# Kernel tuning notes

Measured on AMD Instinct MI355X. Metric: run time of the kernel, lower is better.

The kernel has to match this reference:

```python
import jax, jax.numpy as jnp
import numpy as np
from jax import lax

B, CIN, HIN, WIN = 8, 64, 256, 256
DIM, HEADS, KD, NHKD, D, DH, POS = 128, 8, 8, 64, 16, 128, 16
CQKV = 2 * NHKD + DH  # 256
DN = ('NCHW', 'OIHW', 'NCHW')


def _cbn(x, w, s, b):
    # 1x1 conv (no bias) + eval-mode BN fused into per-channel scale/bias
    y = jnp.einsum('bchw,oc->bohw', x, w)
    return y * s[:, None, None] + b[:, None, None]


def _interp(pos, n):
    # F.interpolate(mode='linear', align_corners=False) == half-pixel linear resize
    return jax.image.resize(pos, (1, pos.shape[1], n), method='linear')


def setup_inputs() -> dict:
    key = jax.random.key(0)
    ks = jax.random.split(key, 40)
    i = [0]
    def nk():
        i[0] += 1
        return ks[i[0] - 1]
    def w(shp, s=0.05):
        return jax.random.normal(nk(), shp, jnp.float32) * s
    def bn(c):
        return (1.0 + 0.1 * jax.random.normal(nk(), (c,), jnp.float32),
                0.1 * jax.random.normal(nk(), (c,), jnp.float32))
    inp = {}
    inp['x'] = jax.random.normal(nk(), (B, CIN, HIN, WIN), jnp.float32)
    inp['bn1_s'], inp['bn1_b'] = bn(DIM)
    inp['fc1_w'] = w((DIM, DIM, 3, 3))
    inp['fc1_b'] = w((DIM,))
    inp['wq'] = w((NHKD, DIM)); inp['bnq_s'], inp['bnq_b'] = bn(NHKD)
    inp['wk'] = w((NHKD, DIM)); inp['bnk_s'], inp['bnk_b'] = bn(NHKD)
    inp['wv'] = w((DH, DIM)); inp['bnv_s'], inp['bnv_b'] = bn(DH)
    inp['pos_rq'] = w((1, NHKD, POS), 1.0)
    inp['pos_rk'] = w((1, NHKD, POS), 1.0)
    inp['pos_cq'] = w((1, NHKD, POS), 1.0)
    inp['pos_ck'] = w((1, NHKD, POS), 1.0)
    inp['wrow'] = w((DH, DH)); inp['bnrow_s'], inp['bnrow_b'] = bn(DH)
    inp['wcol'] = w((DH, DH)); inp['bncol_s'], inp['bncol_b'] = bn(DH)
    inp['wproj'] = w((DIM, DH)); inp['bnproj_s'], inp['bnproj_b'] = bn(DIM)
    inp['wdw'] = w((CQKV, 1, 3, 3)); inp['bndw_s'], inp['bndw_b'] = bn(CQKV)
    inp['wpw'] = w((DIM, CQKV)); inp['bnpw_s'], inp['bnpw_b'] = bn(DIM)
    return inp


def reference(x, bn1_s, bn1_b, fc1_w, fc1_b,
              wq, bnq_s, bnq_b, wk, bnk_s, bnk_b, wv, bnv_s, bnv_b,
              pos_rq, pos_rk, pos_cq, pos_ck,
              wrow, bnrow_s, bnrow_b, wcol, bncol_s, bncol_b,
              wproj, bnproj_s, bnproj_b,
              wdw, bndw_s, bndw_b, wpw, bnpw_s, bnpw_b):
    pad = [(0, 0), (0, 0), (1, 1), (1, 1)]
    # AvgPool2d(3,2,1) with count_include_pad=True, MaxPool2d(3,2,1)
    y_avg = lax.reduce_window(x, 0.0, lax.add, (1, 1, 3, 3), (1, 1, 2, 2), pad) / 9.0
    y_max = lax.reduce_window(x, -jnp.inf, lax.max, (1, 1, 3, 3), (1, 1, 2, 2), pad)
    y = jnp.concatenate([y_avg, y_max], axis=1)  # [B, DIM, H, W]
    # fc1: BN -> Mish -> Conv3x3 (bias) -> Dropout(eval=identity)
    y = y * bn1_s[:, None, None] + bn1_b[:, None, None]
    y = y * jnp.tanh(jax.nn.softplus(y))
    y = lax.conv_general_dilated(y, fc1_w, (1, 1), [(1, 1), (1, 1)], dimension_numbers=DN)
    y = y + fc1_b[:, None, None]
    Bq, _, H, W = y.shape
    # Attention
    q = _cbn(y, wq, bnq_s, bnq_b)   # [B, NHKD, H, W]
    k = _cbn(y, wk, bnk_s, bnk_b)   # [B, NHKD, H, W]
    v = _cbn(y, wv, bnv_s, bnv_b)   # [B, DH, H, W]
    qkv = jnp.concatenate([q, k, v], axis=1)  # [B, CQKV, H, W]
    qkv = lax.conv_general_dilated(qkv, wdw, (1, 1), [(1, 1), (1, 1)],
                                   dimension_numbers=DN, feature_group_count=CQKV)
    qkv = jax.nn.relu(qkv * bndw_s[:, None, None] + bndw_b[:, None, None])
    qkv = _cbn(qkv, wpw, bnpw_s, bnpw_b)  # [B, DIM, H, W]
    scale = KD ** -0.5
    # row attention (squeeze W)
    qr = (q.mean(-1) + _interp(pos_rq, H)).reshape(Bq, HEADS, KD, H)
    kr = (k.mean(-1) + _interp(pos_rk, H)).reshape(Bq, HEADS, KD, H)
    vr = v.mean(-1).reshape(Bq, HEADS, D, H)
    attn_r = jax.nn.softmax(jnp.einsum('bhki,bhkj->bhij', qr, kr) * scale, axis=-1)
    xr = jnp.einsum('bhij,bhdj->bhdi', attn_r, vr).reshape(Bq, DH, H, 1)
    xr = _cbn(jax.nn.relu(xr), wrow, bnrow_s, bnrow_b)
    # column attention (squeeze H)
    qc = (q.mean(-2) + _interp(pos_cq, W)).reshape(Bq, HEADS, KD, W)
    kc = (k.mean(-2) + _interp(pos_ck, W)).reshape(Bq, HEADS, KD, W)
    vc = v.mean(-2).reshape(Bq, HEADS, D, W)
    attn_c = jax.nn.softmax(jnp.einsum('bhki,bhkj->bhij', qc, kc) * scale, axis=-1)
    xc = jnp.einsum('bhij,bhdj->bhdi', attn_c, vc).reshape(Bq, DH, 1, W)
    xc = _cbn(jax.nn.relu(xc), wcol, bncol_s, bncol_b)
    xx = v + xr + xc
    xx = _cbn(jax.nn.relu(xx), wproj, bnproj_s, bnproj_b)
    # h_sigmoid gate * qkv
    return jnp.clip(xx + 3.0, 0.0, 6.0) / 6.0 * qkv
```

## Files before the change

### kernel.cpp

```cpp
#include <hip/hip_runtime.h>
#include <math.h>

#define S 16384
#define HW 128

typedef __attribute__((ext_vector_type(8))) short short8;
typedef __attribute__((ext_vector_type(4))) float f32x4;

__device__ __forceinline__ float mishf(float t) {
    float sp = (t > 20.0f) ? t : __logf(1.0f + __expf(t));
    float e2 = __expf(-2.0f * sp);
    return t * (1.0f - e2) * __builtin_amdgcn_rcpf(1.0f + e2);
}
__device__ __forceinline__ short f2bf(float f) {
    unsigned u = __float_as_uint(f);
    unsigned r = (u + 0x7FFFu + ((u >> 16) & 1u)) >> 16;
    return (short)r;
}
__device__ __forceinline__ float bf2f(short s) {
    unsigned u = ((unsigned)(unsigned short)s) << 16;
    return __uint_as_float(u);
}
__device__ __forceinline__ unsigned packhl(float v) {
    short h = f2bf(v);
    short l = f2bf(v - bf2f(h));
    return (unsigned)(unsigned short)h | ((unsigned)(unsigned short)l << 16);
}
__device__ __forceinline__ void gl_lds16(const void* g, void* l) {
    __builtin_amdgcn_global_load_lds(
        (const __attribute__((address_space(1))) unsigned int*)g,
        (__attribute__((address_space(3))) unsigned int*)l, 16, 0, 0);
}
__device__ __forceinline__ short8 lds_frag(const char* base, int a) {
    int p = a ^ (((a >> 8) & 7) << 4);
    return *(const short8*)(base + p);
}
__device__ __forceinline__ short8 lds_frag128(const char* base, int a) {
    int p = a ^ (((a >> 7) & 7) << 4);
    return *(const short8*)(base + p);
}
__device__ __forceinline__ int swz128(int a) { return a ^ (((a >> 7) & 7) << 4); }
#define MFMA(a, b, c) __builtin_amdgcn_mfma_f32_16x16x32_bf16(a, b, c, 0, 0, 0)

__global__ void prep_kernel(const float* __restrict__ wq, const float* __restrict__ wk, const float* __restrict__ wv,
                            const float* __restrict__ bnq_s, const float* __restrict__ bnq_b,
                            const float* __restrict__ bnk_s, const float* __restrict__ bnk_b,
                            const float* __restrict__ bnv_s, const float* __restrict__ bnv_b,
                            const float* __restrict__ wpw, const float* __restrict__ wproj,
                            const float* __restrict__ wrow, const float* __restrict__ wcol,
                            const float* __restrict__ fc1_w, const float* __restrict__ wdw,
                            short* __restrict__ wqkv_h,
                            float* __restrict__ sqkv, float* __restrict__ bqkv,
                            short* __restrict__ wpw_h,
                            short* __restrict__ wproj_h,
                            float* __restrict__ wrowT, float* __restrict__ wcolT,
                            short* __restrict__ wch,
                            float* __restrict__ wdwT,
                            short* __restrict__ t0ph, short* __restrict__ t0pl) {
    int tid = blockIdx.x * 256 + threadIdx.x;
    if (tid < 256 * 128) {
        int oc = tid >> 7, ic = tid & 127;
        float w = (oc < 64) ? wq[oc * 128 + ic]
                : (oc < 128) ? wk[(oc - 64) * 128 + ic]
                : wv[(oc - 128) * 128 + ic];
        wqkv_h[tid] = f2bf(w);
    }
    if (tid < 256) {
        sqkv[tid] = (tid < 64) ? bnq_s[tid] : (tid < 128) ? bnk_s[tid - 64] : bnv_s[tid - 128];
        bqkv[tid] = (tid < 64) ? bnq_b[tid] : (tid < 128) ? bnk_b[tid - 64] : bnv_b[tid - 128];
    }
    if (tid < 128 * 256) {
        wpw_h[tid] = f2bf(wpw[tid]);
    }
    if (tid < 128 * 128) {
        wproj_h[tid] = f2bf(wproj[tid]);
        int ic = tid >> 7, oc = tid & 127;
        wrowT[tid] = wrow[oc * 128 + ic];
        wcolT[tid] = wcol[oc * 128 + ic];
    }
    if (tid < 9 * 128 * 128) {
        int tap = tid >> 14;
        int oc = (tid >> 7) & 127;
        int ic = tid & 127;
        wch[tid] = f2bf(fc1_w[(oc * 128 + ic) * 9 + tap]);
    }
    if (tid < 9 * 256) {
        int tap = tid / 256, c = tid % 256;
        wdwT[tap * 256 + c] = wdw[c * 9 + tap];
    }
    if (tid < 132096) {
        int bb = tid / 16512;
        int rem = tid - bb * 16512;
        int part = rem / 8256;
        int e = rem - part * 8256;
        short* p = part ? t0pl : t0ph;
        size_t ib = (size_t)bb * 130 * 130 * 128;
        short8 z = (short8){0, 0, 0, 0, 0, 0, 0, 0};
        if (e < 4160) {
            int row = (e < 2080) ? 0 : 129;
            int off = (e % 2080) * 8;
            *(short8*)(p + ib + (size_t)row * 130 * 128 + off) = z;
        } else {
            int e2 = e - 4160;
            int row = 1 + (e2 >> 5);
            int side = (e2 >> 4) & 1;
            int off = (e2 & 15) * 8;
            *(short8*)(p + ib + ((size_t)row * 130 + (side ? 129 : 0)) * 128 + off) = z;
        }
    }
}

__global__ __launch_bounds__(256) void pool_kernel(const float* __restrict__ x,
                                                   const float* __restrict__ s1, const float* __restrict__ b1,
                                                   short* __restrict__ t0ph, short* __restrict__ t0pl) {
    __shared__ unsigned ot[64][132];
    int bx = blockIdx.x;
    int b = blockIdx.y;
    int h = bx >> 1, wh = bx & 1;
    int t = threadIdx.x;
    int wp = t & 31;
    int c8 = t >> 5;
    int w0 = wh * 64 + wp * 2;
    for (int cs = 0; cs < 8; ++cs) {
        int c = cs * 8 + c8;
        const float* xp = x + (size_t)(b * 64 + c) * 65536;
        float vs[3][5], vm[3][5];
        #pragma unroll
        for (int kh = 0; kh < 3; ++kh) {
            int ih = 2 * h + kh - 1;
            bool hok = (unsigned)ih < 256u;
            #pragma unroll
            for (int j = 0; j < 5; ++j) {
                int iw = 2 * w0 - 1 + j;
                bool ok = hok && (unsigned)iw < 256u;
                float v = ok ? xp[ih * 256 + iw] : 0.f;
                vs[kh][j] = ok ? v : 0.f;
                vm[kh][j] = ok ? v : -INFINITY;
            }
        }
        #pragma unroll
        for (int o = 0; o < 2; ++o) {
            float sum = 0.f, mx = -INFINITY;
            #pragma unroll
            for (int kh = 0; kh < 3; ++kh)
                #pragma unroll
                for (int kw = 0; kw < 3; ++kw) {
                    sum += vs[kh][kw + 2 * o];
                    mx = fmaxf(mx, vm[kh][kw + 2 * o]);
                }
            float ta = mishf((sum * (1.f / 9.f)) * s1[c] + b1[c]);
            float tm = mishf(mx * s1[64 + c] + b1[64 + c]);
            ot[wp * 2 + o][c] = packhl(ta);
            ot[wp * 2 + o][64 + c] = packhl(tm);
        }
    }
    __syncthreads();
    size_t rowbase = ((size_t)(b * 130 + h + 1) * 130 + 1 + wh * 64) * 128;
    short* oph = t0ph + rowbase;
    short* opl = t0pl + rowbase;
    for (int idx = t; idx < 64 * 16; idx += 256) {
        int wloc = idx >> 4, co = idx & 15;
        short8 hv, lv;
        #pragma unroll
        for (int j = 0; j < 8; ++j) {
            unsigned u = ot[wloc][co * 8 + j];
            hv[j] = (short)(u & 0xFFFFu);
            lv[j] = (short)(u >> 16);
        }
        *(short8*)(oph + wloc * 128 + co * 8) = hv;
        *(short8*)(opl + wloc * 128 + co * 8) = lv;
    }
}

__global__ __launch_bounds__(512) void convqkv_mfma(const short* __restrict__ t0ph,
                                                    const short* __restrict__ t0pl,
                                                    const short* __restrict__ wch,
                                                    const float* __restrict__ fb,
                                                    const short* __restrict__ wqkv_h,
                                                    const float* __restrict__ sc, const float* __restrict__ bi,
                                                    short* __restrict__ qh, float* __restrict__ rowmean) {
    __shared__ char sm[69632];
    char* smh = sm;
    char* sml = sm + 33792;
    float* rsum = (float*)(sm + 67584);
    int flat = blockIdx.x;
    int b = flat & 7;
    int h = flat >> 3;
    int tid = threadIdx.x, lane = tid & 63, wid = tid >> 6;
    int l15 = lane & 15, l4 = lane >> 4;
    int wrc = wid >> 2;
    int wcc = wid & 3;
    int spbc = wrc * 64 + l15;
    int ocbc = wcc * 32 + l15;
    f32x4 acc[4][2];
    #pragma unroll
    for (int m = 0; m < 4; ++m)
        #pragma unroll
        for (int n = 0; n < 2; ++n) acc[m][n] = (f32x4){0.f, 0.f, 0.f, 0.f};
    for (int kh = 0; kh < 3; ++kh) {
        __syncthreads();
        const char* gh = (const char*)(t0ph + ((size_t)(b * 130 + h + kh) * 130) * 128);
        const char* gl = (const char*)(t0pl + ((size_t)(b * 130 + h + kh) * 130) * 128);
        #pragma unroll
        for (int it = 0; it < 5; ++it) {
            int idx = it * 512 + tid;
            if (idx < 2080) {
                int dl = idx * 16;
                int srcoff = dl ^ (((dl >> 8) & 7) << 4);
                gl_lds16(gh + srcoff, smh + dl);
                gl_lds16(gl + srcoff, sml + dl);
            }
        }
        __syncthreads();
        #pragma unroll
        for (int kw = 0; kw < 3; ++kw) {
            const short* wbh = wch + (size_t)(kh * 3 + kw) * 16384;
            #pragma unroll
            for (int ks = 0; ks < 4; ++ks) {
                int kb = ks * 64 + l4 * 16;
                int kws = ks * 32 + l4 * 8;
                short8 ah[4], bh[2];
                #pragma unroll
                for (int m = 0; m < 4; ++m)
                    ah[m] = lds_frag(smh, ((spbc + m * 16 + kw) << 8) + kb);
                #pragma unroll
                for (int n = 0; n < 2; ++n)
                    bh[n] = *(const short8*)(wbh + (ocbc + n * 16) * 128 + kws);
                #pragma unroll
                for (int m = 0; m < 4; ++m)
                    #pragma unroll
                    for (int n = 0; n < 2; ++n)
                        acc[m][n] = MFMA(ah[m], bh[n], acc[m][n]);
                short8 al[4];
                #pragma unroll
                for (int m = 0; m < 4; ++m)
                    al[m] = lds_frag(sml, ((spbc + m * 16 + kw) << 8) + kb);
                #pragma unroll
                for (int m = 0; m < 4; ++m)
                    #pragma unroll
                    for (int n = 0; n < 2; ++n)
                        acc[m][n] = MFMA(al[m], bh[n], acc[m][n]);
            }
        }
    }
    float fbv[2];
    #pragma unroll
    for (int n = 0; n < 2; ++n) fbv[n] = fb[wcc * 32 + n * 16 + l15];
    rsum[tid] = 0.f;
    __syncthreads();
    short* ahi = (short*)sm;
    short* alo = (short*)(sm + 33792);
    #pragma unroll
    for (int m = 0; m < 4; ++m)
        #pragma unroll
        for (int n = 0; n < 2; ++n)
            #pragma unroll
            for (int r = 0; r < 4; ++r) {
                int px = wrc * 64 + m * 16 + l4 * 4 + r;
                int ocl = wcc * 32 + n * 16 + l15;
                unsigned u = packhl(acc[m][n][r] + fbv[n]);
                ahi[px * 132 + ocl] = (short)(u & 0xFFFFu);
                alo[px * 132 + ocl] = (short)(u >> 16);
            }
    __syncthreads();
    int spbq = wrc * 64 + l15;
    int ocbq = wcc * 64 + l15;
    f32x4 aq[4][4];
    #pragma unroll
    for (int m = 0; m < 4; ++m)
        #pragma unroll
        for (int n = 0; n < 4; ++n) aq[m][n] = (f32x4){0.f, 0.f, 0.f, 0.f};
    #pragma unroll
    for (int ks = 0; ks < 4; ++ks) {
        int k0 = ks * 32 + l4 * 8;
        short8 ah[4], bh[4];
        #pragma unroll
        for (int m = 0; m < 4; ++m) ah[m] = *(const short8*)(ahi + (spbq + m * 16) * 132 + k0);
        #pragma unroll
        for (int n = 0; n < 4; ++n) bh[n] = *(const short8*)(wqkv_h + (size_t)(ocbq + n * 16) * 128 + k0);
        #pragma unroll
        for (int m = 0; m < 4; ++m)
            #pragma unroll
            for (int n = 0; n < 4; ++n) aq[m][n] = MFMA(ah[m], bh[n], aq[m][n]);
        short8 al[4];
        #pragma unroll
        for (int m = 0; m < 4; ++m) al[m] = *(const short8*)(alo + (spbq + m * 16) * 132 + k0);
        #pragma unroll
        for (int m = 0; m < 4; ++m)
            #pragma unroll
            for (int n = 0; n < 4; ++n) aq[m][n] = MFMA(al[m], bh[n], aq[m][n]);
    }
    #pragma unroll
    for (int n = 0; n < 4; ++n) {
        float v = 0.f;
        #pragma unroll
        for (int m = 0; m < 4; ++m)
            #pragma unroll
            for (int r = 0; r < 4; ++r) v += aq[m][n][r];
        v += __shfl_xor(v, 16);
        v += __shfl_xor(v, 32);
        if (l4 == 0) rsum[wrc * 256 + wcc * 64 + n * 16 + l15] = v;
    }
    float s4[4], b4[4];
    #pragma unroll
    for (int n = 0; n < 4; ++n) {
        s4[n] = sc[wcc * 64 + n * 16 + l15];
        b4[n] = bi[wcc * 64 + n * 16 + l15];
    }
    short* rowout = qh + ((size_t)(b * 128 + h) * 128) * 256;
    #pragma unroll
    for (int m = 0; m < 4; ++m)
        #pragma unroll
        for (int n = 0; n < 4; ++n)
            #pragma unroll
            for (int r = 0; r < 4; ++r) {
                int px = wrc * 64 + m * 16 + l4 * 4 + r;
                int oc = wcc * 64 + n * 16 + l15;
                rowout[px * 256 + oc] = f2bf(aq[m][n][r] * s4[n] + b4[n]);
            }
    __syncthreads();
    if (tid < 256)
        rowmean[((size_t)b * 256 + tid) * 128 + h] =
            (rsum[tid] + rsum[256 + tid]) * sc[tid] * (1.f / 128.f) + bi[tid];
}

__global__ __launch_bounds__(256) void colmean_kernel(const short* __restrict__ qh,
                                                      float* __restrict__ colmean) {
    __shared__ float red[8][256];
    int blk = blockIdx.x;
    int b = blk & 7, w = blk >> 3;
    int tid = threadIdx.x;
    int c8g = tid & 31;
    int hs = tid >> 5;
    float a8[8];
    #pragma unroll
    for (int k = 0; k < 8; ++k) a8[k] = 0.f;
    for (int j = 0; j < 16; ++j) {
        int h = hs * 16 + j;
        short8 v = *(const short8*)(qh + ((size_t)((b * 128 + h) * 128 + w)) * 256 + c8g * 8);
        #pragma unroll
        for (int k = 0; k < 8; ++k) a8[k] += bf2f(v[k]);
    }
    #pragma unroll
    for (int k = 0; k < 8; ++k) red[hs][c8g * 8 + k] = a8[k];
    __syncthreads();
    int c = tid;
    float s = 0.f;
    #pragma unroll
    for (int q = 0; q < 8; ++q) s += red[q][c];
    colmean[((size_t)b * 256 + c) * 128 + w] = s * (1.f / 128.f);
}

__global__ __launch_bounds__(512) void dwpw_mfma(const short* __restrict__ qh,
                                                 const float* __restrict__ wdwT,
                                                 const float* __restrict__ ds, const float* __restrict__ db,
                                                 const short* __restrict__ wpw_h,
                                                 const float* __restrict__ sc, const float* __restrict__ bi,
                                                 float* __restrict__ qb) {
    __shared__ char sm[32768];
    char* smh = sm;
    char* sml = sm + 16384;
    int flat = blockIdx.x;
    int b = flat & 7, h = flat >> 3;
    int tid = threadIdx.x, lane = tid & 63, wid = tid >> 6;
    int wr = wid >> 2, wc = wid & 3;
    int l15 = lane & 15, l4 = lane >> 4;
    int spb = wr * 64 + l15;
    int ocb = wc * 32 + l15;
    int wdw_ = tid >> 3;
    int c8t = tid & 7;
    f32x4 acc[4][2];
    #pragma unroll
    for (int m = 0; m < 4; ++m)
        #pragma unroll
        for (int n = 0; n < 2; ++n) acc[m][n] = (f32x4){0.f, 0.f, 0.f, 0.f};

    #pragma unroll 1
    for (int kc = 0; kc < 4; ++kc) {
        __syncthreads();
        int cbase = kc * 64 + c8t * 8;
        #pragma unroll 1
        for (int i = 0; i < 2; ++i) {
            int w = wdw_ * 2 + i;
            float acc8[8];
            #pragma unroll
            for (int k = 0; k < 8; ++k) acc8[k] = 0.f;
            #pragma unroll
            for (int kh = 0; kh < 3; ++kh) {
                int ih = h + kh - 1;
                if ((unsigned)ih >= 128u) continue;
                #pragma unroll
                for (int kw = 0; kw < 3; ++kw) {
                    int iw = w + kw - 1;
                    if ((unsigned)iw >= 128u) continue;
                    short8 v = *(const short8*)(qh + ((size_t)((b * 128 + ih) * 128 + iw)) * 256 + cbase);
                    const float* wp = wdwT + (kh * 3 + kw) * 256 + cbase;
                    #pragma unroll
                    for (int k = 0; k < 8; ++k)
                        acc8[k] += wp[k] * bf2f(v[k]);
                }
            }
            short8 hv, lv;
            #pragma unroll
            for (int k = 0; k < 8; ++k) {
                float v = fmaxf(acc8[k] * ds[cbase + k] + db[cbase + k], 0.f);
                unsigned u = packhl(v);
                hv[k] = (short)(u & 0xFFFFu);
                lv[k] = (short)(u >> 16);
            }
            int a = swz128(w * 128 + c8t * 16);
            *(short8*)(smh + a) = hv;
            *(short8*)(sml + a) = lv;
        }
        __syncthreads();
        #pragma unroll
        for (int ks = 0; ks < 2; ++ks) {
            int kb = ks * 64 + l4 * 16;
            int kws = kc * 64 + ks * 32 + l4 * 8;
            short8 ah[4], bh[2];
            #pragma unroll
            for (int m = 0; m < 4; ++m) ah[m] = lds_frag128(smh, (spb + m * 16) * 128 + kb);
            #pragma unroll
            for (int n = 0; n < 2; ++n) bh[n] = *(const short8*)(wpw_h + (ocb + n * 16) * 256 + kws);
            #pragma unroll
            for (int m = 0; m < 4; ++m)
                #pragma unroll
                for (int n = 0; n < 2; ++n) acc[m][n] = MFMA(ah[m], bh[n], acc[m][n]);
            short8 al[4];
            #pragma unroll
            for (int m = 0; m < 4; ++m) al[m] = lds_frag128(sml, (spb + m * 16) * 128 + kb);
            #pragma unroll
            for (int m = 0; m < 4; ++m)
                #pragma unroll
                for (int n = 0; n < 2; ++n) acc[m][n] = MFMA(al[m], bh[n], acc[m][n]);
        }
    }
    float s4[2], b4[2];
    #pragma unroll
    for (int n = 0; n < 2; ++n) {
        s4[n] = sc[wc * 32 + n * 16 + l15];
        b4[n] = bi[wc * 32 + n * 16 + l15];
    }
    float* rowout = qb + ((size_t)(b * 128 + h) * 128) * 128;
    #pragma unroll
    for (int m = 0; m < 4; ++m)
        #pragma unroll
        for (int n = 0; n < 2; ++n)
            #pragma unroll
            for (int r = 0; r < 4; ++r) {
                int px = wr * 64 + m * 16 + l4 * 4 + r;
                int oc = wc * 32 + n * 16 + l15;
                rowout[px * 128 + oc] = acc[m][n][r] * s4[n] + b4[n];
            }
}

__global__ __launch_bounds__(128) void attn_kernel(const float* __restrict__ rowmean,
                                                   const float* __restrict__ colmean,
                                                   const float* __restrict__ pos_rq, const float* __restrict__ pos_rk,
                                                   const float* __restrict__ pos_cq, const float* __restrict__ pos_ck,
                                                   float* __restrict__ xr_act, float* __restrict__ xc_act) {
    __shared__ float qr[8][128], kr[8][128], vr[16][128];
    int iscol = blockIdx.x >> 6;
    int sub = blockIdx.x & 63;
    int b = sub >> 3, head = sub & 7;
    const float* meanbuf = iscol ? colmean : rowmean;
    const float* posq = iscol ? pos_cq : pos_rq;
    const float* posk = iscol ? pos_ck : pos_rk;
    float* xact = iscol ? xc_act : xr_act;
    int i = threadIdx.x;
    float src = (i + 0.5f) * 0.125f - 0.5f;
    src = fmaxf(src, 0.f);
    int i0 = (int)src;
    if (i0 > 15) i0 = 15;
    float f = src - (float)i0;
    int i1 = (i0 + 1 > 15) ? 15 : i0 + 1;
    const float* mb = meanbuf + (size_t)b * 256 * 128;
    for (int kd = 0; kd < 8; ++kd) {
        int cq = head * 8 + kd;
        qr[kd][i] = mb[cq * 128 + i] + posq[cq * 16 + i0] * (1.f - f) + posq[cq * 16 + i1] * f;
        kr[kd][i] = mb[(64 + cq) * 128 + i] + posk[cq * 16 + i0] * (1.f - f) + posk[cq * 16 + i1] * f;
    }
    for (int d = 0; d < 16; ++d)
        vr[d][i] = mb[(128 + head * 16 + d) * 128 + i];
    __syncthreads();
    float qreg[8];
    #pragma unroll
    for (int kd = 0; kd < 8; ++kd) qreg[kd] = qr[kd][i];
    const float scale = 0.35355339059327373f;
    float m = -INFINITY;
    for (int j = 0; j < 128; ++j) {
        float sj = 0.f;
        #pragma unroll
        for (int kd = 0; kd < 8; ++kd) sj += qreg[kd] * kr[kd][j];
        m = fmaxf(m, sj * scale);
    }
    float denom = 0.f;
    float acc[16];
    #pragma unroll
    for (int d = 0; d < 16; ++d) acc[d] = 0.f;
    for (int j = 0; j < 128; ++j) {
        float sj = 0.f;
        #pragma unroll
        for (int kd = 0; kd < 8; ++kd) sj += qreg[kd] * kr[kd][j];
        float pj = __expf(sj * scale - m);
        denom += pj;
        #pragma unroll
        for (int d = 0; d < 16; ++d) acc[d] += pj * vr[d][j];
    }
    float inv = __builtin_amdgcn_rcpf(denom);
    float* xp = xact + ((size_t)b * 128 + head * 16) * 128;
    for (int d = 0; d < 16; ++d)
        xp[d * 128 + i] = fmaxf(acc[d] * inv, 0.f);
}

__global__ __launch_bounds__(256) void rc_conv_kernel(const float* __restrict__ xr_act, const float* __restrict__ xc_act,
                                                      const float* __restrict__ wrowT, const float* __restrict__ wcolT,
                                                      const float* __restrict__ rs, const float* __restrict__ rb,
                                                      const float* __restrict__ cs, const float* __restrict__ cb,
                                                      float* __restrict__ xrT, float* __restrict__ xcT) {
    __shared__ float4 lds[128][16];
    int blk = blockIdx.x;
    int iscol = blk >> 4;
    int rem = blk & 15;
    int b = rem >> 1;
    int i0 = (rem & 1) * 64;
    const float* src = iscol ? xc_act : xr_act;
    const float* wT  = iscol ? wcolT : wrowT;
    const float* ss  = iscol ? cs : rs;
    const float* sb  = iscol ? cb : rb;
    float* dst       = iscol ? xcT : xrT;
    int tid = threadIdx.x;
    const float4* src4 = (const float4*)(src + (size_t)b * 16384 + i0);
    for (int idx = tid; idx < 128 * 16; idx += 256) {
        int ic = idx >> 4, q = idx & 15;
        lds[ic][q] = src4[ic * 32 + q];
    }
    __syncthreads();
    int oc = tid & 127, sub = tid >> 7;
    float4 acc[8];
    #pragma unroll
    for (int q = 0; q < 8; ++q) acc[q] = make_float4(0.f, 0.f, 0.f, 0.f);
    for (int ic = 0; ic < 128; ++ic) {
        float w = wT[ic * 128 + oc];
        #pragma unroll
        for (int q = 0; q < 8; ++q) {
            float4 v = lds[ic][sub * 8 + q];
            acc[q].x += w * v.x; acc[q].y += w * v.y;
            acc[q].z += w * v.z; acc[q].w += w * v.w;
        }
    }
    float s = ss[oc], bb = sb[oc];
    int ibase = i0 + sub * 32;
    #pragma unroll
    for (int q = 0; q < 8; ++q) {
        float vv[4] = {acc[q].x, acc[q].y, acc[q].z, acc[q].w};
        #pragma unroll
        for (int r = 0; r < 4; ++r) {
            int i = ibase + q * 4 + r;
            dst[((size_t)b * 128 + i) * 128 + oc] = vv[r] * s + bb;
        }
    }
}

__global__ __launch_bounds__(512) void final_mfma(const short* __restrict__ qh,
                                                  const float* __restrict__ xrT, const float* __restrict__ xcT,
                                                  const short* __restrict__ wproj_h,
                                                  const float* __restrict__ ps, const float* __restrict__ pb,
                                                  const float* __restrict__ qb, float* __restrict__ out) {
    __shared__ char sm[69632];
    short* ahi = (short*)sm;
    short* alo = (short*)(sm + 34816);
    int flat = blockIdx.x;
    int b = flat & 7, h = flat >> 3;
    int tid = threadIdx.x, lane = tid & 63, wid = tid >> 6;
    int wr = wid >> 2, wc = wid & 3;
    int l15 = lane & 15, l4 = lane >> 4;
    int spb = wr * 64 + l15;
    int ocb = wc * 32 + l15;
    for (int i = 0; i < 4; ++i) {
        int idx = tid + i * 512;
        int px = idx >> 4, g = idx & 15;
        short8 v8 = *(const short8*)(qh + ((size_t)((b * 128 + h) * 128 + px)) * 256 + 128 + g * 8);
        const float* xr = xrT + ((size_t)(b * 128 + h)) * 128 + g * 8;
        const float* xc = xcT + ((size_t)(b * 128 + px)) * 128 + g * 8;
        short8 hv, lv;
        #pragma unroll
        for (int k = 0; k < 8; ++k) {
            float v = bf2f(v8[k]) + xr[k] + xc[k];
            v = fmaxf(v, 0.f);
            unsigned u = packhl(v);
            hv[k] = (short)(u & 0xFFFFu);
            lv[k] = (short)(u >> 16);
        }
        *(short8*)(ahi + px * 136 + g * 8) = hv;
        *(short8*)(alo + px * 136 + g * 8) = lv;
    }
    __syncthreads();
    f32x4 acc[4][2];
    #pragma unroll
    for (int m = 0; m < 4; ++m)
        #pragma unroll
        for (int n = 0; n < 2; ++n) acc[m][n] = (f32x4){0.f, 0.f, 0.f, 0.f};
    #pragma unroll
    for (int ks = 0; ks < 4; ++ks) {
        int ko = ks * 32 + l4 * 8;
        short8 ah[4], bh[2];
        #pragma unroll
        for (int m = 0; m < 4; ++m) ah[m] = *(const short8*)(ahi + (spb + m * 16) * 136 + ko);
        #pragma unroll
        for (int n = 0; n < 2; ++n) bh[n] = *(const short8*)(wproj_h + (ocb + n * 16) * 128 + ko);
        #pragma unroll
        for (int m = 0; m < 4; ++m)
            #pragma unroll
            for (int n = 0; n < 2; ++n) acc[m][n] = MFMA(ah[m], bh[n], acc[m][n]);
        short8 al[4];
        #pragma unroll
        for (int m = 0; m < 4; ++m) al[m] = *(const short8*)(alo + (spb + m * 16) * 136 + ko);
        #pragma unroll
        for (int m = 0; m < 4; ++m)
            #pragma unroll
            for (int n = 0; n < 2; ++n) acc[m][n] = MFMA(al[m], bh[n], acc[m][n]);
    }
    float s4[2], b4[2];
    #pragma unroll
    for (int n = 0; n < 2; ++n) {
        s4[n] = ps[wc * 32 + n * 16 + l15];
        b4[n] = pb[wc * 32 + n * 16 + l15];
    }
    float* tr = (float*)sm;
    #pragma unroll 1
    for (int p = 0; p < 2; ++p) {
        __syncthreads();
        if ((wc >> 1) == p) {
            #pragma unroll
            for (int n = 0; n < 2; ++n)
                #pragma unroll
                for (int m = 0; m < 4; ++m)
                    #pragma unroll
                    for (int r = 0; r < 4; ++r) {
                        int px = wr * 64 + m * 16 + l4 * 4 + r;
                        int ocl = (wc & 1) * 32 + n * 16 + l15;
                        int oc = p * 64 + ocl;
                        float val = acc[m][n][r] * s4[n] + b4[n];
                        float hs = fminf(fmaxf(val + 3.f, 0.f), 6.f) * (1.f / 6.f);
                        float g = qb[((size_t)((b * 128 + h) * 128 + px)) * 128 + oc];
                        tr[ocl * 129 + px] = hs * g;
                    }
        }
        __syncthreads();
        int ocl = tid >> 3, q = tid & 7;
        int oc = p * 64 + ocl;
        float* yp = out + (size_t)(b * 128 + oc) * S + h * 128 + q * 16;
        #pragma unroll
        for (int j = 0; j < 16; j += 4) {
            float4 v;
            v.x = tr[ocl * 129 + q * 16 + j];
            v.y = tr[ocl * 129 + q * 16 + j + 1];
            v.z = tr[ocl * 129 + q * 16 + j + 2];
            v.w = tr[ocl * 129 + q * 16 + j + 3];
            *(float4*)(yp + j) = v;
        }
    }
}

extern "C" void kernel_launch(void* const* d_in, const int* in_sizes, int n_in,
                              void* d_out, int out_size, void* d_ws, size_t ws_size,
                              hipStream_t stream) {
    const float* x       = (const float*)d_in[0];
    const float* bn1_s   = (const float*)d_in[1];
    const float* bn1_b   = (const float*)d_in[2];
    const float* fc1_w   = (const float*)d_in[3];
    const float* fc1_b   = (const float*)d_in[4];
    const float* wq      = (const float*)d_in[5];
    const float* bnq_s   = (const float*)d_in[6];
    const float* bnq_b   = (const float*)d_in[7];
    const float* wk      = (const float*)d_in[8];
    const float* bnk_s   = (const float*)d_in[9];
    const float* bnk_b   = (const float*)d_in[10];
    const float* wv      = (const float*)d_in[11];
    const float* bnv_s   = (const float*)d_in[12];
    const float* bnv_b   = (const float*)d_in[13];
    const float* pos_rq  = (const float*)d_in[14];
    const float* pos_rk  = (const float*)d_in[15];
    const float* pos_cq  = (const float*)d_in[16];
    const float* pos_ck  = (const float*)d_in[17];
    const float* wrow    = (const float*)d_in[18];
    const float* bnrow_s = (const float*)d_in[19];
    const float* bnrow_b = (const float*)d_in[20];
    const float* wcol    = (const float*)d_in[21];
    const float* bncol_s = (const float*)d_in[22];
    const float* bncol_b = (const float*)d_in[23];
    const float* wproj   = (const float*)d_in[24];
    const float* bnproj_s= (const float*)d_in[25];
    const float* bnproj_b= (const float*)d_in[26];
    const float* wdw     = (const float*)d_in[27];
    const float* bndw_s  = (const float*)d_in[28];
    const float* bndw_b  = (const float*)d_in[29];
    const float* wpw     = (const float*)d_in[30];
    const float* bnpw_s  = (const float*)d_in[31];
    const float* bnpw_b  = (const float*)d_in[32];

    char* ws = (char*)d_ws;
    short* t0ph  = (short*)(ws);
    short* t0pl  = (short*)(ws + (size_t)34611200);
    short* qkvh  = (short*)(ws + (size_t)136331264);
    float* qkvb  = (float*)(ws + (size_t)270548992);
    char* sp = ws + (size_t)337657856;
    float* rowmean = (float*)sp; sp += 1048576;
    float* colmean = (float*)sp; sp += 1048576;
    float* xr_act  = (float*)sp; sp += 524288;
    float* xc_act  = (float*)sp; sp += 524288;
    float* xrT     = (float*)sp; sp += 524288;
    float* xcT     = (float*)sp; sp += 524288;
    short* wch     = (short*)sp; sp += 294912;
    short* wqkv_h  = (short*)sp; sp += 65536;
    short* wpw_h   = (short*)sp; sp += 65536;
    short* wproj_h = (short*)sp; sp += 32768;
    float* wrowT   = (float*)sp; sp += 65536;
    float* wcolT   = (float*)sp; sp += 65536;
    float* sqkv    = (float*)sp; sp += 1024;
    float* bqkv    = (float*)sp; sp += 1024;
    float* wdwT    = (float*)sp; sp += 9216;

    float* out = (float*)d_out;

    prep_kernel<<<576, 256, 0, stream>>>(wq, wk, wv, bnq_s, bnq_b, bnk_s, bnk_b, bnv_s, bnv_b,
                                         wpw, wproj, wrow, wcol, fc1_w, wdw,
                                         wqkv_h, sqkv, bqkv, wpw_h,
                                         wproj_h, wrowT, wcolT, wch, wdwT,
                                         t0ph, t0pl);
    pool_kernel<<<dim3(256, 8), 256, 0, stream>>>(x, bn1_s, bn1_b, t0ph, t0pl);
    convqkv_mfma<<<1024, 512, 0, stream>>>(t0ph, t0pl, wch, fc1_b,
                                           wqkv_h, sqkv, bqkv, qkvh, rowmean);
    colmean_kernel<<<1024, 256, 0, stream>>>(qkvh, colmean);
    dwpw_mfma<<<1024, 512, 0, stream>>>(qkvh, wdwT, bndw_s, bndw_b,
                                        wpw_h, bnpw_s, bnpw_b, qkvb);
    attn_kernel<<<128, 128, 0, stream>>>(rowmean, colmean, pos_rq, pos_rk, pos_cq, pos_ck,
                                         xr_act, xc_act);
    rc_conv_kernel<<<32, 256, 0, stream>>>(xr_act, xc_act, wrowT, wcolT,
                                           bnrow_s, bnrow_b, bncol_s, bncol_b, xrT, xcT);
    final_mfma<<<1024, 512, 0, stream>>>(qkvh, xrT, xcT, wproj_h,
                                         bnproj_s, bnproj_b, qkvb, out);
}
```

Before: 444.8 us.

## Replace split bf16 hi/lo activations with single fp16 MFMA path

Activations were previously stored as two bf16 halves (hi plus residual lo), and every GEMM ran two MFMA passes to emulate higher precision. The activations and weights now use fp16 with the f16 MFMA instruction, which halves the MFMA count, the activation memory traffic and the LDS footprint in the conv, dwpw and final kernels. The cost is lower precision (fp16 mantissa, limited range), which may hurt accuracy against the fp32 reference.

```diff
diff --git a/kernel.cpp b/kernel.cpp
--- a/kernel.cpp
+++ b/kernel.cpp
@@ -5,6 +5,7 @@
 #define HW 128
 
 typedef __attribute__((ext_vector_type(8))) short short8;
+typedef __attribute__((ext_vector_type(8))) _Float16 half8;
 typedef __attribute__((ext_vector_type(4))) float f32x4;
 
 __device__ __forceinline__ float mishf(float t) {
@@ -12,35 +13,25 @@
     float e2 = __expf(-2.0f * sp);
     return t * (1.0f - e2) * __builtin_amdgcn_rcpf(1.0f + e2);
 }
-__device__ __forceinline__ short f2bf(float f) {
-    unsigned u = __float_as_uint(f);
-    unsigned r = (u + 0x7FFFu + ((u >> 16) & 1u)) >> 16;
-    return (short)r;
-}
-__device__ __forceinline__ float bf2f(short s) {
-    unsigned u = ((unsigned)(unsigned short)s) << 16;
-    return __uint_as_float(u);
-}
-__device__ __forceinline__ unsigned packhl(float v) {
-    short h = f2bf(v);
-    short l = f2bf(v - bf2f(h));
-    return (unsigned)(unsigned short)h | ((unsigned)(unsigned short)l << 16);
+__device__ __forceinline__ short f2h(float f) {
+    _Float16 h = (_Float16)f;
+    return __builtin_bit_cast(short, h);
 }
 __device__ __forceinline__ void gl_lds16(const void* g, void* l) {
     __builtin_amdgcn_global_load_lds(
         (const __attribute__((address_space(1))) unsigned int*)g,
         (__attribute__((address_space(3))) unsigned int*)l, 16, 0, 0);
 }
-__device__ __forceinline__ short8 lds_frag(const char* base, int a) {
+__device__ __forceinline__ half8 lds_fragh(const char* base, int a) {
     int p = a ^ (((a >> 8) & 7) << 4);
-    return *(const short8*)(base + p);
-}
-__device__ __forceinline__ short8 lds_frag128(const char* base, int a) {
+    return *(const half8*)(base + p);
+}
+__device__ __forceinline__ half8 lds_frag128h(const char* base, int a) {
     int p = a ^ (((a >> 7) & 7) << 4);
-    return *(const short8*)(base + p);
+    return *(const half8*)(base + p);
 }
 __device__ __forceinline__ int swz128(int a) { return a ^ (((a >> 7) & 7) << 4); }
-#define MFMA(a, b, c) __builtin_amdgcn_mfma_f32_16x16x32_bf16(a, b, c, 0, 0, 0)
+#define MFMA(a, b, c) __builtin_amdgcn_mfma_f32_16x16x32_f16(a, b, c, 0, 0, 0)
 
 __global__ void prep_kernel(const float* __restrict__ wq, const float* __restrict__ wk, const float* __restrict__ wv,
                             const float* __restrict__ bnq_s, const float* __restrict__ bnq_b,
@@ -56,24 +47,24 @@
                             float* __restrict__ wrowT, float* __restrict__ wcolT,
                             short* __restrict__ wch,
                             float* __restrict__ wdwT,
-                            short* __restrict__ t0ph, short* __restrict__ t0pl) {
+                            short* __restrict__ t0p) {
     int tid = blockIdx.x * 256 + threadIdx.x;
     if (tid < 256 * 128) {
         int oc = tid >> 7, ic = tid & 127;
         float w = (oc < 64) ? wq[oc * 128 + ic]
                 : (oc < 128) ? wk[(oc - 64) * 128 + ic]
                 : wv[(oc - 128) * 128 + ic];
-        wqkv_h[tid] = f2bf(w);
+        wqkv_h[tid] = f2h(w);
     }
     if (tid < 256) {
         sqkv[tid] = (tid < 64) ? bnq_s[tid] : (tid < 128) ? bnk_s[tid - 64] : bnv_s[tid - 128];
         bqkv[tid] = (tid < 64) ? bnq_b[tid] : (tid < 128) ? bnk_b[tid - 64] : bnv_b[tid - 128];
     }
     if (tid < 128 * 256) {
-        wpw_h[tid] = f2bf(wpw[tid]);
+        wpw_h[tid] = f2h(wpw[tid]);
     }
     if (tid < 128 * 128) {
-        wproj_h[tid] = f2bf(wproj[tid]);
+        wproj_h[tid] = f2h(wproj[tid]);
         int ic = tid >> 7, oc = tid & 127;
         wrowT[tid] = wrow[oc * 128 + ic];
         wcolT[tid] = wcol[oc * 128 + ic];
@@ -82,38 +73,35 @@
         int tap = tid >> 14;
         int oc = (tid >> 7) & 127;
         int ic = tid & 127;
-        wch[tid] = f2bf(fc1_w[(oc * 128 + ic) * 9 + tap]);
+        wch[tid] = f2h(fc1_w[(oc * 128 + ic) * 9 + tap]);
     }
     if (tid < 9 * 256) {
         int tap = tid / 256, c = tid % 256;
         wdwT[tap * 256 + c] = wdw[c * 9 + tap];
     }
-    if (tid < 132096) {
-        int bb = tid / 16512;
-        int rem = tid - bb * 16512;
-        int part = rem / 8256;
-        int e = rem - part * 8256;
-        short* p = part ? t0pl : t0ph;
+    if (tid < 66048) {
+        int bb = tid / 8256;
+        int e = tid - bb * 8256;
         size_t ib = (size_t)bb * 130 * 130 * 128;
         short8 z = (short8){0, 0, 0, 0, 0, 0, 0, 0};
         if (e < 4160) {
             int row = (e < 2080) ? 0 : 129;
             int off = (e % 2080) * 8;
-            *(short8*)(p + ib + (size_t)row * 130 * 128 + off) = z;
+            *(short8*)(t0p + ib + (size_t)row * 130 * 128 + off) = z;
         } else {
             int e2 = e - 4160;
             int row = 1 + (e2 >> 5);
             int side = (e2 >> 4) & 1;
             int off = (e2 & 15) * 8;
-            *(short8*)(p + ib + ((size_t)row * 130 + (side ? 129 : 0)) * 128 + off) = z;
+            *(short8*)(t0p + ib + ((size_t)row * 130 + (side ? 129 : 0)) * 128 + off) = z;
         }
     }
 }
 
 __global__ __launch_bounds__(256) void pool_kernel(const float* __restrict__ x,
                                                    const float* __restrict__ s1, const float* __restrict__ b1,
-                                                   short* __restrict__ t0ph, short* __restrict__ t0pl) {
-    __shared__ unsigned ot[64][132];
+                                                   short* __restrict__ t0p) {
+    __shared__ short ot[64][136];
     int bx = blockIdx.x;
     int b = blockIdx.y;
     int h = bx >> 1, wh = bx & 1;
@@ -150,39 +138,28 @@
                 }
             float ta = mishf((sum * (1.f / 9.f)) * s1[c] + b1[c]);
             float tm = mishf(mx * s1[64 + c] + b1[64 + c]);
-            ot[wp * 2 + o][c] = packhl(ta);
-            ot[wp * 2 + o][64 + c] = packhl(tm);
+            ot[wp * 2 + o][c] = f2h(ta);
+            ot[wp * 2 + o][64 + c] = f2h(tm);
         }
     }
     __syncthreads();
     size_t rowbase = ((size_t)(b * 130 + h + 1) * 130 + 1 + wh * 64) * 128;
-    short* oph = t0ph + rowbase;
-    short* opl = t0pl + rowbase;
+    short* op = t0p + rowbase;
     for (int idx = t; idx < 64 * 16; idx += 256) {
         int wloc = idx >> 4, co = idx & 15;
-        short8 hv, lv;
-        #pragma unroll
-        for (int j = 0; j < 8; ++j) {
-            unsigned u = ot[wloc][co * 8 + j];
-            hv[j] = (short)(u & 0xFFFFu);
-            lv[j] = (short)(u >> 16);
-        }
-        *(short8*)(oph + wloc * 128 + co * 8) = hv;
-        *(short8*)(opl + wloc * 128 + co * 8) = lv;
-    }
-}
-
-__global__ __launch_bounds__(512) void convqkv_mfma(const short* __restrict__ t0ph,
-                                                    const short* __restrict__ t0pl,
+        short8 v = *(const short8*)(&ot[wloc][co * 8]);
+        *(short8*)(op + wloc * 128 + co * 8) = v;
+    }
+}
+
+__global__ __launch_bounds__(512) void convqkv_mfma(const short* __restrict__ t0p,
                                                     const short* __restrict__ wch,
                                                     const float* __restrict__ fb,
                                                     const short* __restrict__ wqkv_h,
                                                     const float* __restrict__ sc, const float* __restrict__ bi,
                                                     short* __restrict__ qh, float* __restrict__ rowmean) {
-    __shared__ char sm[69632];
-    char* smh = sm;
-    char* sml = sm + 33792;
-    float* rsum = (float*)(sm + 67584);
+    __shared__ char sm[35840];
+    float* rsum = (float*)(sm + 33792);
     int flat = blockIdx.x;
     int b = flat & 7;
     int h = flat >> 3;
@@ -199,16 +176,14 @@
         for (int n = 0; n < 2; ++n) acc[m][n] = (f32x4){0.f, 0.f, 0.f, 0.f};
     for (int kh = 0; kh < 3; ++kh) {
         __syncthreads();
-        const char* gh = (const char*)(t0ph + ((size_t)(b * 130 + h + kh) * 130) * 128);
-        const char* gl = (const char*)(t0pl + ((size_t)(b * 130 + h + kh) * 130) * 128);
+        const char* gp = (const char*)(t0p + ((size_t)(b * 130 + h + kh) * 130) * 128);
         #pragma unroll
         for (int it = 0; it < 5; ++it) {
             int idx = it * 512 + tid;
             if (idx < 2080) {
                 int dl = idx * 16;
                 int srcoff = dl ^ (((dl >> 8) & 7) << 4);
-                gl_lds16(gh + srcoff, smh + dl);
-                gl_lds16(gl + srcoff, sml + dl);
+                gl_lds16(gp + srcoff, sm + dl);
             }
         }
         __syncthreads();
@@ -219,27 +194,18 @@
             for (int ks = 0; ks < 4; ++ks) {
                 int kb = ks * 64 + l4 * 16;
                 int kws = ks * 32 + l4 * 8;
-                short8 ah[4], bh[2];
+                half8 ah[4], bh[2];
                 #pragma unroll
                 for (int m = 0; m < 4; ++m)
-                    ah[m] = lds_frag(smh, ((spbc + m * 16 + kw) << 8) + kb);
+                    ah[m] = lds_fragh(sm, ((spbc + m * 16 + kw) << 8) + kb);
                 #pragma unroll
                 for (int n = 0; n < 2; ++n)
-                    bh[n] = *(const short8*)(wbh + (ocbc + n * 16) * 128 + kws);
+                    bh[n] = *(const half8*)(wbh + (ocbc + n * 16) * 128 + kws);
                 #pragma unroll
                 for (int m = 0; m < 4; ++m)
                     #pragma unroll
                     for (int n = 0; n < 2; ++n)
                         acc[m][n] = MFMA(ah[m], bh[n], acc[m][n]);
-                short8 al[4];
-                #pragma unroll
-                for (int m = 0; m < 4; ++m)
-                    al[m] = lds_frag(sml, ((spbc + m * 16 + kw) << 8) + kb);
-                #pragma unroll
-                for (int m = 0; m < 4; ++m)
-                    #pragma unroll
-                    for (int n = 0; n < 2; ++n)
-                        acc[m][n] = MFMA(al[m], bh[n], acc[m][n]);
             }
         }
     }
@@ -248,8 +214,7 @@
     for (int n = 0; n < 2; ++n) fbv[n] = fb[wcc * 32 + n * 16 + l15];
     rsum[tid] = 0.f;
     __syncthreads();
-    short* ahi = (short*)sm;
-    short* alo = (short*)(sm + 33792);
+    short* ap = (short*)sm;
     #pragma unroll
     for (int m = 0; m < 4; ++m)
         #pragma unroll
@@ -258,9 +223,7 @@
             for (int r = 0; r < 4; ++r) {
                 int px = wrc * 64 + m * 16 + l4 * 4 + r;
                 int ocl = wcc * 32 + n * 16 + l15;
-                unsigned u = packhl(acc[m][n][r] + fbv[n]);
-                ahi[px * 132 + ocl] = (short)(u & 0xFFFFu);
-                alo[px * 132 + ocl] = (short)(u >> 16);
+                ap[px * 132 + ocl] = f2h(acc[m][n][r] + fbv[n]);
             }
     __syncthreads();
     int spbq = wrc * 64 + l15;
@@ -273,22 +236,15 @@
     #pragma unroll
     for (int ks = 0; ks < 4; ++ks) {
         int k0 = ks * 32 + l4 * 8;
-        short8 ah[4], bh[4];
-        #pragma unroll
-        for (int m = 0; m < 4; ++m) ah[m] = *(const short8*)(ahi + (spbq + m * 16) * 132 + k0);
-        #pragma unroll
-        for (int n = 0; n < 4; ++n) bh[n] = *(const short8*)(wqkv_h + (size_t)(ocbq + n * 16) * 128 + k0);
+        half8 ah[4], bh[4];
+        #pragma unroll
+        for (int m = 0; m < 4; ++m) ah[m] = *(const half8*)(ap + (spbq + m * 16) * 132 + k0);
+        #pragma unroll
+        for (int n = 0; n < 4; ++n) bh[n] = *(const half8*)(wqkv_h + (size_t)(ocbq + n * 16) * 128 + k0);
         #pragma unroll
         for (int m = 0; m < 4; ++m)
             #pragma unroll
             for (int n = 0; n < 4; ++n) aq[m][n] = MFMA(ah[m], bh[n], aq[m][n]);
-        short8 al[4];
-        #pragma unroll
-        for (int m = 0; m < 4; ++m) al[m] = *(const short8*)(alo + (spbq + m * 16) * 132 + k0);
-        #pragma unroll
-        for (int m = 0; m < 4; ++m)
-            #pragma unroll
-            for (int n = 0; n < 4; ++n) aq[m][n] = MFMA(al[m], bh[n], aq[m][n]);
     }
     #pragma unroll
     for (int n = 0; n < 4; ++n) {
@@ -316,7 +272,7 @@
             for (int r = 0; r < 4; ++r) {
                 int px = wrc * 64 + m * 16 + l4 * 4 + r;
                 int oc = wcc * 64 + n * 16 + l15;
-                rowout[px * 256 + oc] = f2bf(aq[m][n][r] * s4[n] + b4[n]);
+                rowout[px * 256 + oc] = f2h(aq[m][n][r] * s4[n] + b4[n]);
             }
     __syncthreads();
     if (tid < 256)
@@ -337,9 +293,9 @@
     for (int k = 0; k < 8; ++k) a8[k] = 0.f;
     for (int j = 0; j < 16; ++j) {
         int h = hs * 16 + j;
-        short8 v = *(const short8*)(qh + ((size_t)((b * 128 + h) * 128 + w)) * 256 + c8g * 8);
-        #pragma unroll
-        for (int k = 0; k < 8; ++k) a8[k] += bf2f(v[k]);
+        half8 v = *(const half8*)(qh + ((size_t)((b * 128 + h) * 128 + w)) * 256 + c8g * 8);
+        #pragma unroll
+        for (int k = 0; k < 8; ++k) a8[k] += (float)v[k];
     }
     #pragma unroll
     for (int k = 0; k < 8; ++k) red[hs][c8g * 8 + k] = a8[k];
@@ -357,9 +313,7 @@
                                                  const short* __restrict__ wpw_h,
                                                  const float* __restrict__ sc, const float* __restrict__ bi,
                                                  float* __restrict__ qb) {
-    __shared__ char sm[32768];
-    char* smh = sm;
-    char* sml = sm + 16384;
+    __shared__ char sm[16384];
     int flat = blockIdx.x;
     int b = flat & 7, h = flat >> 3;
     int tid = threadIdx.x, lane = tid & 63, wid = tid >> 6;
@@ -393,46 +347,35 @@
                 for (int kw = 0; kw < 3; ++kw) {
                     int iw = w + kw - 1;
                     if ((unsigned)iw >= 128u) continue;
-                    short8 v = *(const short8*)(qh + ((size_t)((b * 128 + ih) * 128 + iw)) * 256 + cbase);
+                    half8 v = *(const half8*)(qh + ((size_t)((b * 128 + ih) * 128 + iw)) * 256 + cbase);
                     const float* wp = wdwT + (kh * 3 + kw) * 256 + cbase;
                     #pragma unroll
                     for (int k = 0; k < 8; ++k)
-                        acc8[k] += wp[k] * bf2f(v[k]);
+                        acc8[k] += wp[k] * (float)v[k];
                 }
             }
-            short8 hv, lv;
+            short8 hv;
             #pragma unroll
             for (int k = 0; k < 8; ++k) {
                 float v = fmaxf(acc8[k] * ds[cbase + k] + db[cbase + k], 0.f);
-                unsigned u = packhl(v);
-                hv[k] = (short)(u & 0xFFFFu);
-                lv[k] = (short)(u >> 16);
-            }
-            int a = swz128(w * 128 + c8t * 16);
-            *(short8*)(smh + a) = hv;
-            *(short8*)(sml + a) = lv;
+                hv[k] = f2h(v);
+            }
+            *(short8*)(sm + swz128(w * 128 + c8t * 16)) = hv;
         }
         __syncthreads();
         #pragma unroll
         for (int ks = 0; ks < 2; ++ks) {
             int kb = ks * 64 + l4 * 16;
             int kws = kc * 64 + ks * 32 + l4 * 8;
-            short8 ah[4], bh[2];
-            #pragma unroll
-            for (int m = 0; m < 4; ++m) ah[m] = lds_frag128(smh, (spb + m * 16) * 128 + kb);
-            #pragma unroll
-            for (int n = 0; n < 2; ++n) bh[n] = *(const short8*)(wpw_h + (ocb + n * 16) * 256 + kws);
+            half8 ah[4], bh[2];
+            #pragma unroll
+            for (int m = 0; m < 4; ++m) ah[m] = lds_frag128h(sm, (spb + m * 16) * 128 + kb);
+            #pragma unroll
+            for (int n = 0; n < 2; ++n) bh[n] = *(const half8*)(wpw_h + (ocb + n * 16) * 256 + kws);
             #pragma unroll
             for (int m = 0; m < 4; ++m)
                 #pragma unroll
                 for (int n = 0; n < 2; ++n) acc[m][n] = MFMA(ah[m], bh[n], acc[m][n]);
-            short8 al[4];
-            #pragma unroll
-            for (int m = 0; m < 4; ++m) al[m] = lds_frag128(sml, (spb + m * 16) * 128 + kb);
-            #pragma unroll
-            for (int m = 0; m < 4; ++m)
-                #pragma unroll
-                for (int n = 0; n < 2; ++n) acc[m][n] = MFMA(al[m], bh[n], acc[m][n]);
         }
     }
     float s4[2], b4[2];
@@ -567,9 +510,8 @@
                                                   const short* __restrict__ wproj_h,
                                                   const float* __restrict__ ps, const float* __restrict__ pb,
                                                   const float* __restrict__ qb, float* __restrict__ out) {
-    __shared__ char sm[69632];
-    short* ahi = (short*)sm;
-    short* alo = (short*)(sm + 34816);
+    __shared__ char sm[34816];
+    short* ap = (short*)sm;
     int flat = blockIdx.x;
     int b = flat & 7, h = flat >> 3;
     int tid = threadIdx.x, lane = tid & 63, wid = tid >> 6;
@@ -580,20 +522,16 @@
     for (int i = 0; i < 4; ++i) {
         int idx = tid + i * 512;
         int px = idx >> 4, g = idx & 15;
-        short8 v8 = *(const short8*)(qh + ((size_t)((b * 128 + h) * 128 + px)) * 256 + 128 + g * 8);
+        half8 v8 = *(const half8*)(qh + ((size_t)((b * 128 + h) * 128 + px)) * 256 + 128 + g * 8);
         const float* xr = xrT + ((size_t)(b * 128 + h)) * 128 + g * 8;
         const float* xc = xcT + ((size_t)(b * 128 + px)) * 128 + g * 8;
-        short8 hv, lv;
+        short8 hv;
         #pragma unroll
         for (int k = 0; k < 8; ++k) {
-            float v = bf2f(v8[k]) + xr[k] + xc[k];
-            v = fmaxf(v, 0.f);
-            unsigned u = packhl(v);
-            hv[k] = (short)(u & 0xFFFFu);
-            lv[k] = (short)(u >> 16);
-        }
-        *(short8*)(ahi + px * 136 + g * 8) = hv;
-        *(short8*)(alo + px * 136 + g * 8) = lv;
+            float v = (float)v8[k] + xr[k] + xc[k];
+            hv[k] = f2h(fmaxf(v, 0.f));
+        }
+        *(short8*)(ap + px * 136 + g * 8) = hv;
     }
     __syncthreads();
     f32x4 acc[4][2];
@@ -604,22 +542,15 @@
     #pragma unroll
     for (int ks = 0; ks < 4; ++ks) {
         int ko = ks * 32 + l4 * 8;
-        short8 ah[4], bh[2];
-        #pragma unroll
-        for (int m = 0; m < 4; ++m) ah[m] = *(const short8*)(ahi + (spb + m * 16) * 136 + ko);
-        #pragma unroll
-        for (int n = 0; n < 2; ++n) bh[n] = *(const short8*)(wproj_h + (ocb + n * 16) * 128 + ko);
+        half8 ah[4], bh[2];
+        #pragma unroll
+        for (int m = 0; m < 4; ++m) ah[m] = *(const half8*)(ap + (spb + m * 16) * 136 + ko);
+        #pragma unroll
+        for (int n = 0; n < 2; ++n) bh[n] = *(const half8*)(wproj_h + (ocb + n * 16) * 128 + ko);
         #pragma unroll
         for (int m = 0; m < 4; ++m)
             #pragma unroll
             for (int n = 0; n < 2; ++n) acc[m][n] = MFMA(ah[m], bh[n], acc[m][n]);
-        short8 al[4];
-        #pragma unroll
-        for (int m = 0; m < 4; ++m) al[m] = *(const short8*)(alo + (spb + m * 16) * 136 + ko);
-        #pragma unroll
-        for (int m = 0; m < 4; ++m)
-            #pragma unroll
-            for (int n = 0; n < 2; ++n) acc[m][n] = MFMA(al[m], bh[n], acc[m][n]);
     }
     float s4[2], b4[2];
     #pragma unroll
@@ -701,8 +632,7 @@
     const float* bnpw_b  = (const float*)d_in[32];
 
     char* ws = (char*)d_ws;
-    short* t0ph  = (short*)(ws);
-    short* t0pl  = (short*)(ws + (size_t)34611200);
+    short* t0p   = (short*)(ws);
     short* qkvh  = (short*)(ws + (size_t)136331264);
     float* qkvb  = (float*)(ws + (size_t)270548992);
     char* sp = ws + (size_t)337657856;
@@ -728,9 +658,9 @@
                                          wpw, wproj, wrow, wcol, fc1_w, wdw,
                                          wqkv_h, sqkv, bqkv, wpw_h,
                                          wproj_h, wrowT, wcolT, wch, wdwT,
-                                         t0ph, t0pl);
-    pool_kernel<<<dim3(256, 8), 256, 0, stream>>>(x, bn1_s, bn1_b, t0ph, t0pl);
-    convqkv_mfma<<<1024, 512, 0, stream>>>(t0ph, t0pl, wch, fc1_b,
+                                         t0p);
+    pool_kernel<<<dim3(256, 8), 256, 0, stream>>>(x, bn1_s, bn1_b, t0p);
+    convqkv_mfma<<<1024, 512, 0, stream>>>(t0p, wch, fc1_b,
                                            wqkv_h, sqkv, bqkv, qkvh, rowmean);
     colmean_kernel<<<1024, 256, 0, stream>>>(qkvh, colmean);
     dwpw_mfma<<<1024, 512, 0, stream>>>(qkvh, wdwT, bndw_s, bndw_b,
```

Result: faster. 391.2 us (-12.0%).
